# Performance work log

Hardware: AMD Instinct MI355X
Metric: run time of the kernel (lower is better)

The kernel has to match this reference:

```python
import jax, jax.numpy as jnp
import numpy as np

N = 10000      # nodes
DEG = 8        # avg out-degree before symmetrization
B = 2          # batch
T = 8          # time steps
F_IN = 1
HID = 64       # spatial hidden = temporal hidden
K = 2          # power-conv hops


def setup_inputs() -> dict:
    rng = np.random.default_rng(0)
    # random sparse adjacency, symmetrized by concatenating reversed edges
    s0 = rng.integers(0, N, size=N * DEG)
    d0 = rng.integers(0, N, size=N * DEG)
    src = np.concatenate([s0, d0]).astype(np.int32)   # [E], E = 2*N*DEG
    dst = np.concatenate([d0, s0]).astype(np.int32)
    vals = np.ones(src.shape[0], np.float32)
    # symmetric normalization: A_hat = D^{-1/2} A D^{-1/2}
    deg = np.zeros(N, np.float32)
    np.add.at(deg, dst, vals)
    dinv = 1.0 / np.sqrt(np.maximum(deg, 1.0))
    vals = (dinv[src] * dinv[dst] * vals).astype(np.float32)

    key = jax.random.key(0)
    ks = jax.random.split(key, 12)
    sc = 0.05
    return {
        "x": jax.random.normal(ks[0], (B, N, T), jnp.float32),
        "edge_src": jnp.asarray(src),
        "edge_dst": jnp.asarray(dst),
        "edge_val": jnp.asarray(vals),
        # PowerGConvDyn layer 1: F_in -> HID, K+1 power weights
        "W_sp1": jax.random.normal(ks[1], (K + 1, F_IN, HID), jnp.float32) * sc,
        "b_sp1": jnp.zeros((HID,), jnp.float32),
        # PowerGConvDyn layer 2: HID -> HID
        "W_sp2": jax.random.normal(ks[2], (K + 1, HID, HID), jnp.float32) * sc,
        "b_sp2": jnp.zeros((HID,), jnp.float32),
        # GRU (torch layout: gates stacked r,z,n)
        "W_ih": jax.random.normal(ks[3], (3 * HID, HID), jnp.float32) * sc,
        "W_hh": jax.random.normal(ks[4], (3 * HID, HID), jnp.float32) * sc,
        "b_ih": jnp.zeros((3 * HID,), jnp.float32),
        "b_hh": jnp.zeros((3 * HID,), jnp.float32),
        # head
        "W_head": jax.random.normal(ks[5], (HID, 1), jnp.float32) * sc,
        "b_head": jnp.zeros((1,), jnp.float32),
    }


def reference(x, edge_src, edge_dst, edge_val,
              W_sp1, b_sp1, W_sp2, b_sp2,
              W_ih, W_hh, b_ih, b_hh, W_head, b_head):
    Bb, Nn, Tt = x.shape
    # batch all (b,t) slices as columns: [N, B*T, F_in]
    H = x.transpose(1, 0, 2).reshape(Nn, Bb * Tt, 1)

    def spmm(Z):  # A_hat @ Z on node axis; Z: [N, M, F]
        msgs = edge_val[:, None, None] * Z[edge_src]           # [E, M, F]
        return jax.ops.segment_sum(msgs, edge_dst, num_segments=Nn)

    def power_layer(Hin, W, b):  # out = sum_k (A^k H) W_k + b, then ReLU
        out = jnp.einsum('nmf,fo->nmo', Hin, W[0])
        Z = Hin
        for k in range(1, W.shape[0]):
            Z = spmm(Z)
            out = out + jnp.einsum('nmf,fo->nmo', Z, W[k])
        return jax.nn.relu(out + b)

    H = power_layer(H, W_sp1, b_sp1)   # [N, B*T, HID]
    H = power_layer(H, W_sp2, b_sp2)   # [N, B*T, HID]
    C = H.shape[-1]

    # [N, B*T, C] -> [T, B*N, C] sequences for the GRU
    Hs = H.reshape(Nn, Bb, Tt, C).transpose(2, 1, 0, 3).reshape(Tt, Bb * Nn, C)

    Hh = W_hh.shape[1]
    h0 = jnp.zeros((Bb * Nn, Hh), x.dtype)

    def gru_step(h, xt):
        gx = xt @ W_ih.T + b_ih
        gh = h @ W_hh.T + b_hh
        rx, zx, nx = jnp.split(gx, 3, axis=-1)
        rh, zh, nh = jnp.split(gh, 3, axis=-1)
        r = jax.nn.sigmoid(rx + rh)
        z = jax.nn.sigmoid(zx + zh)
        n = jnp.tanh(nx + r * nh)
        h = (1.0 - z) * n + z * h
        return h, None

    h_last, _ = jax.lax.scan(gru_step, h0, Hs)   # [B*N, HID]
    y = (h_last @ W_head + b_head).reshape(Bb, Nn)
    return y
```

## Files before the change

kernel.cpp:

```cpp
#include <hip/hip_runtime.h>
#include <math.h>

#define N_NODES 10000
#define B_SZ 2
#define T_STEPS 8
#define M_COLS 16
#define BN 20000
#define NM 160000

typedef __attribute__((ext_vector_type(8))) short short8;
typedef __attribute__((ext_vector_type(4))) float f32x4;

__device__ __forceinline__ float b2f(unsigned short u) {
  union { unsigned int i; float f; } x; x.i = ((unsigned int)u) << 16; return x.f;
}
__device__ __forceinline__ unsigned short f2b(float f) {
  unsigned int x = __float_as_uint(f);
  return (unsigned short)((x + 0x7fffu + ((x >> 16) & 1u)) >> 16);
}
__device__ __forceinline__ float sigm(float x) {
  return 1.f / (1.f + __expf(-x));
}
__device__ __forceinline__ float tanhfast(float x) {
  float xm = fmaxf(x, -15.f);
  float e = __expf(-2.f * xm);
  return (1.f - e) / (1.f + e);
}

__global__ __launch_bounds__(256) void k_count(const int* __restrict__ dst, int* __restrict__ cnt, int E) {
  int e = blockIdx.x*256 + threadIdx.x;
  if (e < E) atomicAdd(&cnt[dst[e]], 1);
}

__global__ __launch_bounds__(256) void k_scan(const int* __restrict__ cnt, int* __restrict__ rowp, int n) {
  const int K = 40;
  int t = threadIdx.x;
  int beg = t*K;
  int end = beg + K < n ? beg + K : n;
  int s = 0;
  for (int i = beg; i < end; ++i) s += cnt[i];
  int lane = t & 63, w = t >> 6;
  int v = s;
#pragma unroll
  for (int off = 1; off < 64; off <<= 1) {
    int u = __shfl_up(v, off, 64);
    if (lane >= off) v += u;
  }
  __shared__ int wsum[4];
  if (lane == 63) wsum[w] = v;
  __syncthreads();
  int woff = 0;
  for (int i = 0; i < w; ++i) woff += wsum[i];
  int run = woff + v - s;
  for (int i = beg; i < end; ++i) { rowp[i] = run; run += cnt[i]; }
  if (t == 255) rowp[n] = run;
}

__global__ __launch_bounds__(256) void k_fill(const int* __restrict__ src, const int* __restrict__ dst,
                                              const float* __restrict__ val, const int* __restrict__ rowp,
                                              int* __restrict__ cur, int* __restrict__ csrs,
                                              float* __restrict__ csrv, int E) {
  int e = blockIdx.x*256 + threadIdx.x;
  if (e >= E) return;
  int d = dst[e];
  int p = atomicAdd(&cur[d], 1);
  int slot = rowp[d] + p;
  csrs[slot] = src[e];
  csrv[slot] = val[e];
}

__global__ __launch_bounds__(256) void k_prep(const float* __restrict__ Wih, const float* __restrict__ W2,
                                              const float* __restrict__ Whh,
                                              unsigned short* __restrict__ Wbih,
                                              unsigned short* __restrict__ W2t,
                                              unsigned short* __restrict__ Whi,
                                              unsigned short* __restrict__ Wlo) {
  int i = blockIdx.x*256 + threadIdx.x;
  if (i >= 12288) return;
  Wbih[i] = f2b(Wih[i]);
  int p = i >> 12, rem = i & 4095, c = rem >> 6, k = rem & 63;
  W2t[i] = f2b(W2[p*4096 + k*64 + c]);
  float v = Whh[i];
  unsigned short h = f2b(v);
  Whi[i] = h;
  Wlo[i] = f2b(v - b2f(h));
}

__global__ __launch_bounds__(256) void k_spmmA(const float* __restrict__ x, float* __restrict__ Z1,
                                               const int* __restrict__ rowp, const int* __restrict__ csrs,
                                               const float* __restrict__ csrv) {
  int i = blockIdx.x*256 + threadIdx.x;
  int n = i >> 4, m = i & 15;
  int b = m >> 3, t = m & 7;
  int s = rowp[n], e = rowp[n+1];
  const float* xb = x + b*(N_NODES*T_STEPS) + t;
  float acc = 0.f;
  for (int k = s; k < e; ++k)
    acc = fmaf(csrv[k], xb[csrs[k]*T_STEPS], acc);
  Z1[i] = acc;
}

__global__ __launch_bounds__(256) void k_spmmB_l1(const float* __restrict__ x, const float* __restrict__ Z1,
                                                  const int* __restrict__ rowp, const int* __restrict__ csrs,
                                                  const float* __restrict__ csrv,
                                                  const float* __restrict__ W1, const float* __restrict__ b1,
                                                  unsigned short* __restrict__ H1b) {
  int i = blockIdx.x*256 + threadIdx.x;
  int n = i >> 4, m = i & 15;
  int b = m >> 3, t = m & 7;
  int s = rowp[n], e = rowp[n+1];
  float z2 = 0.f;
  for (int k = s; k < e; ++k)
    z2 = fmaf(csrv[k], Z1[csrs[k]*16 + m], z2);
  float z0 = x[b*(N_NODES*T_STEPS) + n*T_STEPS + t];
  float z1 = Z1[i];
  unsigned short* dst = H1b + (size_t)i*64;
  union { uint4 v; unsigned short s[8]; } o;
#pragma unroll
  for (int g = 0; g < 8; ++g) {
#pragma unroll
    for (int j = 0; j < 8; ++j) {
      int c = g*8 + j;
      float v = fmaf(z0, W1[c], fmaf(z1, W1[64+c], fmaf(z2, W1[128+c], b1[c])));
      o.s[j] = f2b(v > 0.f ? v : 0.f);
    }
    ((uint4*)dst)[g] = o.v;
  }
}

__global__ __launch_bounds__(256) void k_spmmC(const unsigned short* __restrict__ Zin,
                                               unsigned short* __restrict__ Zout,
                                               const int* __restrict__ rowp, const int* __restrict__ csrs,
                                               const float* __restrict__ csrv) {
  int c = blockIdx.x & 7;
  int grp = blockIdx.x >> 3;
  int n = grp*16 + (threadIdx.x >> 4);
  int l = threadIdx.x & 15;
  int off = c*128 + l*8;
  int s = rowp[n], e = rowp[n+1];
  float acc[8] = {0,0,0,0,0,0,0,0};
  for (int k = s; k < e; ++k) {
    int src = csrs[k];
    float v = csrv[k];
    union { uint4 u; unsigned short s[8]; } z;
    z.u = *(const uint4*)(Zin + (size_t)src*1024 + off);
#pragma unroll
    for (int j = 0; j < 8; ++j) acc[j] = fmaf(v, b2f(z.s[j]), acc[j]);
  }
  union { uint4 u; unsigned short s[8]; } o;
#pragma unroll
  for (int j = 0; j < 8; ++j) o.s[j] = f2b(acc[j]);
  *(uint4*)(Zout + (size_t)n*1024 + off) = o.u;
}

__global__ __launch_bounds__(256) void k_layer2m(const unsigned short* __restrict__ H1b,
                                                 const unsigned short* __restrict__ Z1b,
                                                 const unsigned short* __restrict__ Z2b,
                                                 const unsigned short* __restrict__ Wt,
                                                 const float* __restrict__ b2,
                                                 unsigned short* __restrict__ OUT2b) {
  int wid = blockIdx.x*4 + (threadIdx.x >> 6);
  int lane = threadIdx.x & 63;
  int lr = lane & 15, hi = lane >> 4;
  int rowbase = wid*16;
  const short* A0 = (const short*)H1b + (size_t)(rowbase + lr)*64;
  const short* A1 = (const short*)Z1b + (size_t)(rowbase + lr)*64;
  const short* A2 = (const short*)Z2b + (size_t)(rowbase + lr)*64;
  short8 a[3][2];
  a[0][0] = *(const short8*)(A0 + hi*8); a[0][1] = *(const short8*)(A0 + 32 + hi*8);
  a[1][0] = *(const short8*)(A1 + hi*8); a[1][1] = *(const short8*)(A1 + 32 + hi*8);
  a[2][0] = *(const short8*)(A2 + hi*8); a[2][1] = *(const short8*)(A2 + 32 + hi*8);
  const short* Bp = (const short*)Wt;
  f32x4 acc[4];
#pragma unroll
  for (int ct = 0; ct < 4; ++ct) {
    int col = ct*16 + lr;
    f32x4 c = {0.f, 0.f, 0.f, 0.f};
#pragma unroll
    for (int p = 0; p < 3; ++p) {
      short8 b0 = *(const short8*)(Bp + p*4096 + col*64 + hi*8);
      short8 b1 = *(const short8*)(Bp + p*4096 + col*64 + 32 + hi*8);
      c = __builtin_amdgcn_mfma_f32_16x16x32_bf16(a[p][0], b0, c, 0, 0, 0);
      c = __builtin_amdgcn_mfma_f32_16x16x32_bf16(a[p][1], b1, c, 0, 0, 0);
    }
    acc[ct] = c;
  }
#pragma unroll
  for (int ct = 0; ct < 4; ++ct) {
    int col = ct*16 + lr;
    float bb = b2[col];
#pragma unroll
    for (int r = 0; r < 4; ++r) {
      int nm = rowbase + hi*4 + r;
      int n = nm >> 4, m = nm & 15;
      int bi = m >> 3, t = m & 7;
      float v = acc[ct][r] + bb;
      OUT2b[((size_t)((t*2 + bi)*N_NODES + n))*64 + col] = f2b(v > 0.f ? v : 0.f);
    }
  }
}

__global__ __launch_bounds__(256, 1) void k_gru(const unsigned short* __restrict__ OUT2b,
                                                const unsigned short* __restrict__ Whhi,
                                                const unsigned short* __restrict__ Whlo,
                                                const unsigned short* __restrict__ Wihb,
                                                const float* __restrict__ bih,
                                                const float* __restrict__ bhh,
                                                const float* __restrict__ Whead,
                                                const float* __restrict__ bhead,
                                                float* __restrict__ y) {
  extern __shared__ char smem[];
  uint4* WF = (uint4*)smem;
  float* HSb = (float*)(smem + 73728);
  int tid = threadIdx.x;
  for (int idx = tid; idx < 72*64; idx += 256) {
    int f = idx >> 6, ln = idx & 63;
    int lrr = ln & 15, h4r = ln >> 4;
    int g = (f < 24) ? f : ((f < 48) ? f - 24 : f - 48);
    int ct = g >> 1, kc = g & 1;
    const unsigned short* src = (f < 24) ? Whhi : ((f < 48) ? Whlo : Wihb);
    WF[idx] = *(const uint4*)(src + (ct*16 + lrr)*64 + kc*32 + h4r*8);
  }
  int w = tid >> 6, lane = tid & 63;
  int lr = lane & 15, h4 = lane >> 4;
  float* hs = HSb + w*(16*68);
  for (int i = lane; i < 16*68; i += 64) hs[i] = 0.f;
  __syncthreads();
  int Wv = blockIdx.x*4 + w;
  if (Wv >= 1250) return;
  int base = Wv*16;
  int row0 = base + lr;
  int b0 = row0 >= N_NODES ? 1 : 0;
  int n0 = row0 - b0*N_NODES;

  float cR[4], cZ[4], bNi[4], bNh[4];
#pragma unroll
  for (int cr = 0; cr < 4; ++cr) {
    int col = cr*16 + lr;
    cR[cr]  = bih[col] + bhh[col];
    cZ[cr]  = bih[64+col] + bhh[64+col];
    bNi[cr] = bih[128+col];
    bNh[cr] = bhh[128+col];
  }
  float hreg[4][4];
#pragma unroll
  for (int cr = 0; cr < 4; ++cr)
#pragma unroll
    for (int j = 0; j < 4; ++j) hreg[cr][j] = 0.f;
  const short* O = (const short*)OUT2b;

#pragma unroll 1
  for (int t = 0; t < 8; ++t) {
    short8 ax[2];
    size_t ab0 = ((size_t)((t*2 + b0)*N_NODES + n0))*64;
#pragma unroll
    for (int kc = 0; kc < 2; ++kc)
      ax[kc] = *(const short8*)(O + ab0 + kc*32 + h4*8);
    short8 ahi[2], alo[2];
#pragma unroll
    for (int kc = 0; kc < 2; ++kc) {
      const float* hp = hs + lr*68 + kc*32 + h4*8;
      float4 v0 = *(const float4*)hp;
      float4 v1 = *(const float4*)(hp + 4);
      float hv[8];
      hv[0]=v0.x; hv[1]=v0.y; hv[2]=v0.z; hv[3]=v0.w;
      hv[4]=v1.x; hv[5]=v1.y; hv[6]=v1.z; hv[7]=v1.w;
      union { short8 v; unsigned short s[8]; } uh, ul;
#pragma unroll
      for (int j = 0; j < 8; ++j) {
        unsigned short hb = (unsigned short)(__float_as_uint(hv[j]) >> 16);
        uh.s[j] = hb;
        ul.s[j] = f2b(hv[j] - b2f(hb));
      }
      ahi[kc] = uh.v; alo[kc] = ul.v;
    }
    f32x4 aR[4], aZ[4], aNx[4], aNh[4];
#pragma unroll
    for (int cr = 0; cr < 4; ++cr) {
      f32x4 zz = {0.f,0.f,0.f,0.f};
      aR[cr] = zz; aZ[cr] = zz; aNx[cr] = zz; aNh[cr] = zz;
    }
#pragma unroll
    for (int ct = 0; ct < 12; ++ct) {
#pragma unroll
      for (int kc = 0; kc < 2; ++kc) {
        short8 bhi = *(const short8*)&WF[(ct*2 + kc)*64 + lane];
        short8 blo = *(const short8*)&WF[(24 + ct*2 + kc)*64 + lane];
        short8 bx  = *(const short8*)&WF[(48 + ct*2 + kc)*64 + lane];
        if (ct < 4) {
          aR[ct] = __builtin_amdgcn_mfma_f32_16x16x32_bf16(ax[kc],  bx,  aR[ct], 0, 0, 0);
          aR[ct] = __builtin_amdgcn_mfma_f32_16x16x32_bf16(ahi[kc], bhi, aR[ct], 0, 0, 0);
          aR[ct] = __builtin_amdgcn_mfma_f32_16x16x32_bf16(ahi[kc], blo, aR[ct], 0, 0, 0);
          aR[ct] = __builtin_amdgcn_mfma_f32_16x16x32_bf16(alo[kc], bhi, aR[ct], 0, 0, 0);
        } else if (ct < 8) {
          int cc = ct - 4;
          aZ[cc] = __builtin_amdgcn_mfma_f32_16x16x32_bf16(ax[kc],  bx,  aZ[cc], 0, 0, 0);
          aZ[cc] = __builtin_amdgcn_mfma_f32_16x16x32_bf16(ahi[kc], bhi, aZ[cc], 0, 0, 0);
          aZ[cc] = __builtin_amdgcn_mfma_f32_16x16x32_bf16(ahi[kc], blo, aZ[cc], 0, 0, 0);
          aZ[cc] = __builtin_amdgcn_mfma_f32_16x16x32_bf16(alo[kc], bhi, aZ[cc], 0, 0, 0);
        } else {
          int cc = ct - 8;
          aNx[cc] = __builtin_amdgcn_mfma_f32_16x16x32_bf16(ax[kc],  bx,  aNx[cc], 0, 0, 0);
          aNh[cc] = __builtin_amdgcn_mfma_f32_16x16x32_bf16(ahi[kc], bhi, aNh[cc], 0, 0, 0);
          aNh[cc] = __builtin_amdgcn_mfma_f32_16x16x32_bf16(ahi[kc], blo, aNh[cc], 0, 0, 0);
          aNh[cc] = __builtin_amdgcn_mfma_f32_16x16x32_bf16(alo[kc], bhi, aNh[cc], 0, 0, 0);
        }
      }
    }
#pragma unroll
    for (int cr = 0; cr < 4; ++cr)
#pragma unroll
      for (int j = 0; j < 4; ++j) {
        float r = sigm(aR[cr][j] + cR[cr]);
        float z = sigm(aZ[cr][j] + cZ[cr]);
        float nn = tanhfast(aNx[cr][j] + bNi[cr] + r*(aNh[cr][j] + bNh[cr]));
        float hv = (1.f - z)*nn + z*hreg[cr][j];
        hreg[cr][j] = hv;
        hs[(h4*4 + j)*68 + cr*16 + lr] = hv;
      }
  }
  float wv[4];
#pragma unroll
  for (int cr = 0; cr < 4; ++cr) wv[cr] = Whead[cr*16 + lr];
#pragma unroll
  for (int j = 0; j < 4; ++j) {
    float p = 0.f;
#pragma unroll
    for (int cr = 0; cr < 4; ++cr) p = fmaf(hreg[j >= 0 ? cr : 0][j], wv[cr], p);
#pragma unroll
    for (int off = 1; off <= 8; off <<= 1)
      p += __shfl_xor(p, off, 64);
    if (lr == 0) y[base + h4*4 + j] = p + bhead[0];
  }
}

extern "C" void kernel_launch(void* const* d_in, const int* in_sizes, int n_in,
                              void* d_out, int out_size, void* d_ws, size_t ws_size,
                              hipStream_t stream) {
  const float* x    = (const float*)d_in[0];
  const int*   esrc = (const int*)d_in[1];
  const int*   edst = (const int*)d_in[2];
  const float* eval = (const float*)d_in[3];
  const float* W1   = (const float*)d_in[4];
  const float* b1   = (const float*)d_in[5];
  const float* W2   = (const float*)d_in[6];
  const float* b2   = (const float*)d_in[7];
  const float* Wih  = (const float*)d_in[8];
  const float* Whh  = (const float*)d_in[9];
  const float* bih  = (const float*)d_in[10];
  const float* bhh  = (const float*)d_in[11];
  const float* Whead= (const float*)d_in[12];
  const float* bhead= (const float*)d_in[13];
  int E = in_sizes[1];
  float* y = (float*)d_out;

  char* wsb = (char*)d_ws;
  unsigned short* H1b   = (unsigned short*)(wsb + 0);
  unsigned short* ZB1   = (unsigned short*)(wsb + 20480000);
  unsigned short* ZB2   = (unsigned short*)(wsb + 40960000);
  unsigned short* OUT2b = (unsigned short*)(wsb + 61440000);
  float* Z1   = (float*)(wsb + 82560000);
  int*   rowp = (int*)(wsb + 83840000);
  int*   cnt  = (int*)(wsb + 83880064);
  int*   csrs = (int*)(wsb + 83920064);
  float* csrv = (float*)(wsb + 84560064);
  unsigned short* Wbih = (unsigned short*)(wsb + 85200064);
  unsigned short* W2t  = (unsigned short*)(wsb + 85224640);
  unsigned short* Whhi = (unsigned short*)(wsb + 85249280);
  unsigned short* Whlo = (unsigned short*)(wsb + 85273856);

  int eb = (E + 255) / 256;

  hipMemsetAsync(cnt, 0, N_NODES*sizeof(int), stream);
  k_count<<<eb, 256, 0, stream>>>(edst, cnt, E);
  k_scan<<<1, 256, 0, stream>>>(cnt, rowp, N_NODES);
  hipMemsetAsync(cnt, 0, N_NODES*sizeof(int), stream);
  k_fill<<<eb, 256, 0, stream>>>(esrc, edst, eval, rowp, cnt, csrs, csrv, E);
  k_prep<<<48, 256, 0, stream>>>(Wih, W2, Whh, Wbih, W2t, Whhi, Whlo);

  k_spmmA<<<625, 256, 0, stream>>>(x, Z1, rowp, csrs, csrv);
  k_spmmB_l1<<<625, 256, 0, stream>>>(x, Z1, rowp, csrs, csrv, W1, b1, H1b);

  k_spmmC<<<5000, 256, 0, stream>>>(H1b, ZB1, rowp, csrs, csrv);
  k_spmmC<<<5000, 256, 0, stream>>>(ZB1, ZB2, rowp, csrs, csrv);
  k_layer2m<<<2500, 256, 0, stream>>>(H1b, ZB1, ZB2, W2t, b2, OUT2b);

  const int gru_lds = 73728 + 4*16*68*4;
  hipFuncSetAttribute((const void*)k_gru, hipFuncAttributeMaxDynamicSharedMemorySize, gru_lds);
  k_gru<<<313, 256, gru_lds, stream>>>(OUT2b, Whhi, Whlo, Wbih, bih, bhh, Whead, bhead, y);
}
```

Measured before the change: 270.5 us.

## Split GRU gates across three waves per 16-row tile with register-resident W_hh

The GRU kernel now gives each 16-row tile its own 192-thread block. Each of the three waves computes one gate (r, z or n), instead of one wave computing all three gates for its rows. The recurrent weight hi/lo fragments stay in registers, so only W_ih goes to LDS, which cuts LDS use and lets more blocks run per CU. The r and z pre-activations are exchanged through LDS to the n-gate wave, which does the nonlinearity and state update. This costs two block barriers per time step, and two of the three waves sit idle during the elementwise phase.

```diff
diff --git a/kernel.cpp b/kernel.cpp
--- a/kernel.cpp
+++ b/kernel.cpp
@@ -200,7 +200,7 @@
   }
 }
 
-__global__ __launch_bounds__(256, 1) void k_gru(const unsigned short* __restrict__ OUT2b,
+__global__ __launch_bounds__(192, 2) void k_gru(const unsigned short* __restrict__ OUT2b,
                                                 const unsigned short* __restrict__ Whhi,
                                                 const unsigned short* __restrict__ Whlo,
                                                 const unsigned short* __restrict__ Wihb,
@@ -210,37 +210,41 @@
                                                 const float* __restrict__ bhead,
                                                 float* __restrict__ y) {
   extern __shared__ char smem[];
-  uint4* WF = (uint4*)smem;
-  float* HSb = (float*)(smem + 73728);
+  uint4* WX  = (uint4*)smem;
+  float* hs  = (float*)(smem + 24576);
+  float* gex = (float*)(smem + 24576 + 4864);
   int tid = threadIdx.x;
-  for (int idx = tid; idx < 72*64; idx += 256) {
+  for (int idx = tid; idx < 24*64; idx += 192) {
     int f = idx >> 6, ln = idx & 63;
     int lrr = ln & 15, h4r = ln >> 4;
-    int g = (f < 24) ? f : ((f < 48) ? f - 24 : f - 48);
-    int ct = g >> 1, kc = g & 1;
-    const unsigned short* src = (f < 24) ? Whhi : ((f < 48) ? Whlo : Wihb);
-    WF[idx] = *(const uint4*)(src + (ct*16 + lrr)*64 + kc*32 + h4r*8);
-  }
-  int w = tid >> 6, lane = tid & 63;
-  int lr = lane & 15, h4 = lane >> 4;
-  float* hs = HSb + w*(16*68);
-  for (int i = lane; i < 16*68; i += 64) hs[i] = 0.f;
-  __syncthreads();
-  int Wv = blockIdx.x*4 + w;
-  if (Wv >= 1250) return;
-  int base = Wv*16;
+    int ct = f >> 1, kc = f & 1;
+    WX[idx] = *(const uint4*)(Wihb + (ct*16 + lrr)*64 + kc*32 + h4r*8);
+  }
+  for (int i = tid; i < 16*76; i += 192) hs[i] = 0.f;
+  int w = __builtin_amdgcn_readfirstlane(tid >> 6);
+  int lane = tid & 63, lr = lane & 15, h4 = lane >> 4;
+  int base = blockIdx.x*16;
   int row0 = base + lr;
   int b0 = row0 >= N_NODES ? 1 : 0;
   int n0 = row0 - b0*N_NODES;
 
-  float cR[4], cZ[4], bNi[4], bNh[4];
+  const unsigned short* Whp = Whhi;
+  const unsigned short* Wlp = Whlo;
+  short8 wh[4][2], wl[4][2];
+#pragma unroll
+  for (int ct = 0; ct < 4; ++ct)
+#pragma unroll
+    for (int kc = 0; kc < 2; ++kc) {
+      int col = w*64 + ct*16 + lr;
+      wh[ct][kc] = *(const short8*)((const short*)Whp + col*64 + kc*32 + h4*8);
+      wl[ct][kc] = *(const short8*)((const short*)Wlp + col*64 + kc*32 + h4*8);
+    }
+  float c0[4], c1[4];
 #pragma unroll
   for (int cr = 0; cr < 4; ++cr) {
-    int col = cr*16 + lr;
-    cR[cr]  = bih[col] + bhh[col];
-    cZ[cr]  = bih[64+col] + bhh[64+col];
-    bNi[cr] = bih[128+col];
-    bNh[cr] = bhh[128+col];
+    int col = w*64 + cr*16 + lr;
+    if (w < 2) { c0[cr] = bih[col] + bhh[col]; c1[cr] = 0.f; }
+    else       { c0[cr] = bih[col];            c1[cr] = bhh[col]; }
   }
   float hreg[4][4];
 #pragma unroll
@@ -248,18 +252,25 @@
 #pragma unroll
     for (int j = 0; j < 4; ++j) hreg[cr][j] = 0.f;
   const short* O = (const short*)OUT2b;
+  __syncthreads();
 
 #pragma unroll 1
   for (int t = 0; t < 8; ++t) {
+#pragma unroll
+    for (int ct = 0; ct < 4; ++ct)
+#pragma unroll
+      for (int kc = 0; kc < 2; ++kc) {
+        asm volatile("" : "+v"(wh[ct][kc]));
+        asm volatile("" : "+v"(wl[ct][kc]));
+      }
     short8 ax[2];
     size_t ab0 = ((size_t)((t*2 + b0)*N_NODES + n0))*64;
-#pragma unroll
-    for (int kc = 0; kc < 2; ++kc)
-      ax[kc] = *(const short8*)(O + ab0 + kc*32 + h4*8);
+    ax[0] = *(const short8*)(O + ab0 + h4*8);
+    ax[1] = *(const short8*)(O + ab0 + 32 + h4*8);
     short8 ahi[2], alo[2];
 #pragma unroll
     for (int kc = 0; kc < 2; ++kc) {
-      const float* hp = hs + lr*68 + kc*32 + h4*8;
+      const float* hp = hs + lr*76 + kc*32 + h4*8;
       float4 v0 = *(const float4*)hp;
       float4 v1 = *(const float4*)(hp + 4);
       float hv[8];
@@ -274,63 +285,70 @@
       }
       ahi[kc] = uh.v; alo[kc] = ul.v;
     }
-    f32x4 aR[4], aZ[4], aNx[4], aNh[4];
+    f32x4 accA[4], accB[4];
 #pragma unroll
     for (int cr = 0; cr < 4; ++cr) {
       f32x4 zz = {0.f,0.f,0.f,0.f};
-      aR[cr] = zz; aZ[cr] = zz; aNx[cr] = zz; aNh[cr] = zz;
-    }
-#pragma unroll
-    for (int ct = 0; ct < 12; ++ct) {
+      accA[cr] = zz; accB[cr] = zz;
+    }
+#pragma unroll
+    for (int ct = 0; ct < 4; ++ct) {
 #pragma unroll
       for (int kc = 0; kc < 2; ++kc) {
-        short8 bhi = *(const short8*)&WF[(ct*2 + kc)*64 + lane];
-        short8 blo = *(const short8*)&WF[(24 + ct*2 + kc)*64 + lane];
-        short8 bx  = *(const short8*)&WF[(48 + ct*2 + kc)*64 + lane];
-        if (ct < 4) {
-          aR[ct] = __builtin_amdgcn_mfma_f32_16x16x32_bf16(ax[kc],  bx,  aR[ct], 0, 0, 0);
-          aR[ct] = __builtin_amdgcn_mfma_f32_16x16x32_bf16(ahi[kc], bhi, aR[ct], 0, 0, 0);
-          aR[ct] = __builtin_amdgcn_mfma_f32_16x16x32_bf16(ahi[kc], blo, aR[ct], 0, 0, 0);
-          aR[ct] = __builtin_amdgcn_mfma_f32_16x16x32_bf16(alo[kc], bhi, aR[ct], 0, 0, 0);
-        } else if (ct < 8) {
-          int cc = ct - 4;
-          aZ[cc] = __builtin_amdgcn_mfma_f32_16x16x32_bf16(ax[kc],  bx,  aZ[cc], 0, 0, 0);
-          aZ[cc] = __builtin_amdgcn_mfma_f32_16x16x32_bf16(ahi[kc], bhi, aZ[cc], 0, 0, 0);
-          aZ[cc] = __builtin_amdgcn_mfma_f32_16x16x32_bf16(ahi[kc], blo, aZ[cc], 0, 0, 0);
-          aZ[cc] = __builtin_amdgcn_mfma_f32_16x16x32_bf16(alo[kc], bhi, aZ[cc], 0, 0, 0);
+        short8 bx = *(const short8*)&WX[(w*8 + ct*2 + kc)*64 + lane];
+        if (w < 2) {
+          accA[ct] = __builtin_amdgcn_mfma_f32_16x16x32_bf16(ax[kc],  bx,         accA[ct], 0, 0, 0);
+          accA[ct] = __builtin_amdgcn_mfma_f32_16x16x32_bf16(ahi[kc], wh[ct][kc], accA[ct], 0, 0, 0);
+          accA[ct] = __builtin_amdgcn_mfma_f32_16x16x32_bf16(ahi[kc], wl[ct][kc], accA[ct], 0, 0, 0);
+          accA[ct] = __builtin_amdgcn_mfma_f32_16x16x32_bf16(alo[kc], wh[ct][kc], accA[ct], 0, 0, 0);
         } else {
-          int cc = ct - 8;
-          aNx[cc] = __builtin_amdgcn_mfma_f32_16x16x32_bf16(ax[kc],  bx,  aNx[cc], 0, 0, 0);
-          aNh[cc] = __builtin_amdgcn_mfma_f32_16x16x32_bf16(ahi[kc], bhi, aNh[cc], 0, 0, 0);
-          aNh[cc] = __builtin_amdgcn_mfma_f32_16x16x32_bf16(ahi[kc], blo, aNh[cc], 0, 0, 0);
-          aNh[cc] = __builtin_amdgcn_mfma_f32_16x16x32_bf16(alo[kc], bhi, aNh[cc], 0, 0, 0);
+          accA[ct] = __builtin_amdgcn_mfma_f32_16x16x32_bf16(ax[kc],  bx,         accA[ct], 0, 0, 0);
+          accB[ct] = __builtin_amdgcn_mfma_f32_16x16x32_bf16(ahi[kc], wh[ct][kc], accB[ct], 0, 0, 0);
+          accB[ct] = __builtin_amdgcn_mfma_f32_16x16x32_bf16(ahi[kc], wl[ct][kc], accB[ct], 0, 0, 0);
+          accB[ct] = __builtin_amdgcn_mfma_f32_16x16x32_bf16(alo[kc], wh[ct][kc], accB[ct], 0, 0, 0);
         }
       }
     }
-#pragma unroll
-    for (int cr = 0; cr < 4; ++cr)
-#pragma unroll
-      for (int j = 0; j < 4; ++j) {
-        float r = sigm(aR[cr][j] + cR[cr]);
-        float z = sigm(aZ[cr][j] + cZ[cr]);
-        float nn = tanhfast(aNx[cr][j] + bNi[cr] + r*(aNh[cr][j] + bNh[cr]));
-        float hv = (1.f - z)*nn + z*hreg[cr][j];
-        hreg[cr][j] = hv;
-        hs[(h4*4 + j)*68 + cr*16 + lr] = hv;
-      }
-  }
-  float wv[4];
-#pragma unroll
-  for (int cr = 0; cr < 4; ++cr) wv[cr] = Whead[cr*16 + lr];
-#pragma unroll
-  for (int j = 0; j < 4; ++j) {
-    float p = 0.f;
-#pragma unroll
-    for (int cr = 0; cr < 4; ++cr) p = fmaf(hreg[j >= 0 ? cr : 0][j], wv[cr], p);
-#pragma unroll
-    for (int off = 1; off <= 8; off <<= 1)
-      p += __shfl_xor(p, off, 64);
-    if (lr == 0) y[base + h4*4 + j] = p + bhead[0];
+    if (w < 2) {
+#pragma unroll
+      for (int cr = 0; cr < 4; ++cr)
+#pragma unroll
+        for (int j = 0; j < 4; ++j)
+          gex[(w*16 + cr*4 + j)*64 + lane] = accA[cr][j] + c0[cr];
+    }
+    __syncthreads();
+    if (w == 2) {
+#pragma unroll
+      for (int cr = 0; cr < 4; ++cr)
+#pragma unroll
+        for (int j = 0; j < 4; ++j) {
+          float rv = gex[(cr*4 + j)*64 + lane];
+          float zv = gex[(16 + cr*4 + j)*64 + lane];
+          float r = sigm(rv);
+          float z = sigm(zv);
+          float nn = tanhfast(accA[cr][j] + c0[cr] + r*(accB[cr][j] + c1[cr]));
+          float hv = (1.f - z)*nn + z*hreg[cr][j];
+          hreg[cr][j] = hv;
+          hs[(h4*4 + j)*76 + cr*16 + lr] = hv;
+        }
+    }
+    __syncthreads();
+  }
+  if (w == 2) {
+    float wv[4];
+#pragma unroll
+    for (int cr = 0; cr < 4; ++cr) wv[cr] = Whead[cr*16 + lr];
+#pragma unroll
+    for (int j = 0; j < 4; ++j) {
+      float p = 0.f;
+#pragma unroll
+      for (int cr = 0; cr < 4; ++cr) p = fmaf(hreg[cr][j], wv[cr], p);
+      p += __shfl_xor(p, 1, 64);
+      p += __shfl_xor(p, 2, 64);
+      p += __shfl_xor(p, 4, 64);
+      p += __shfl_xor(p, 8, 64);
+      if (lr == 0) y[base + h4*4 + j] = p + bhead[0];
+    }
   }
 }
 
@@ -385,7 +403,7 @@
   k_spmmC<<<5000, 256, 0, stream>>>(ZB1, ZB2, rowp, csrs, csrv);
   k_layer2m<<<2500, 256, 0, stream>>>(H1b, ZB1, ZB2, W2t, b2, OUT2b);
 
-  const int gru_lds = 73728 + 4*16*68*4;
+  const int gru_lds = 24576 + 16*76*4 + 2*16*64*4;
   hipFuncSetAttribute((const void*)k_gru, hipFuncAttributeMaxDynamicSharedMemorySize, gru_lds);
-  k_gru<<<313, 256, gru_lds, stream>>>(OUT2b, Whhi, Whlo, Wbih, bih, bhh, Whead, bhead, y);
-}
+  k_gru<<<1250, 192, gru_lds, stream>>>(OUT2b, Whhi, Whlo, Wbih, bih, bhh, Whead, bhead, y);
+}
```

Result: slower. 292.7 us (+8.2%).

## Enlarge GRU blocks to 12 waves, keep input weights in registers, fuse memset into scan

Applied to the files above, without the earlier changes.

The GRU kernel now runs 768-thread blocks (12 waves) instead of 4 waves. The W_ih bf16 fragments move from LDS into per-lane registers, which shrinks the LDS weight region so more waves share one copy of W_hh hi/lo. The second memset of the counter array is folded into the scan kernel, removing one API call. The hi part of the hidden-state split now uses round-to-nearest instead of truncation, and the head reduction loop is written out by hand. Holding 24 short8 weight fragments per lane raises register pressure and may hurt occupancy or cause spills; the grid also drops to 105 blocks.

```diff
diff --git a/kernel.cpp b/kernel.cpp
--- a/kernel.cpp
+++ b/kernel.cpp
@@ -32,13 +32,14 @@
   if (e < E) atomicAdd(&cnt[dst[e]], 1);
 }
 
-__global__ __launch_bounds__(256) void k_scan(const int* __restrict__ cnt, int* __restrict__ rowp, int n) {
+__global__ __launch_bounds__(256) void k_scan(const int* __restrict__ cntin, int* __restrict__ rowp,
+                                              int* __restrict__ cntz, int n) {
   const int K = 40;
   int t = threadIdx.x;
   int beg = t*K;
   int end = beg + K < n ? beg + K : n;
   int s = 0;
-  for (int i = beg; i < end; ++i) s += cnt[i];
+  for (int i = beg; i < end; ++i) s += cntin[i];
   int lane = t & 63, w = t >> 6;
   int v = s;
 #pragma unroll
@@ -52,7 +53,11 @@
   int woff = 0;
   for (int i = 0; i < w; ++i) woff += wsum[i];
   int run = woff + v - s;
-  for (int i = beg; i < end; ++i) { rowp[i] = run; run += cnt[i]; }
+  for (int i = beg; i < end; ++i) {
+    rowp[i] = run;
+    run += cntin[i];
+    cntz[i] = 0;
+  }
   if (t == 255) rowp[n] = run;
 }
 
@@ -200,7 +205,7 @@
   }
 }
 
-__global__ __launch_bounds__(256, 1) void k_gru(const unsigned short* __restrict__ OUT2b,
+__global__ __launch_bounds__(768, 3) void k_gru(const unsigned short* __restrict__ OUT2b,
                                                 const unsigned short* __restrict__ Whhi,
                                                 const unsigned short* __restrict__ Whlo,
                                                 const unsigned short* __restrict__ Wihb,
@@ -211,14 +216,14 @@
                                                 float* __restrict__ y) {
   extern __shared__ char smem[];
   uint4* WF = (uint4*)smem;
-  float* HSb = (float*)(smem + 73728);
+  float* HSb = (float*)(smem + 49152);
   int tid = threadIdx.x;
-  for (int idx = tid; idx < 72*64; idx += 256) {
+  for (int idx = tid; idx < 48*64; idx += 768) {
     int f = idx >> 6, ln = idx & 63;
     int lrr = ln & 15, h4r = ln >> 4;
-    int g = (f < 24) ? f : ((f < 48) ? f - 24 : f - 48);
+    int g = (f < 24) ? f : f - 24;
     int ct = g >> 1, kc = g & 1;
-    const unsigned short* src = (f < 24) ? Whhi : ((f < 48) ? Whlo : Wihb);
+    const unsigned short* src = (f < 24) ? Whhi : Whlo;
     WF[idx] = *(const uint4*)(src + (ct*16 + lrr)*64 + kc*32 + h4r*8);
   }
   int w = tid >> 6, lane = tid & 63;
@@ -226,12 +231,20 @@
   float* hs = HSb + w*(16*68);
   for (int i = lane; i < 16*68; i += 64) hs[i] = 0.f;
   __syncthreads();
-  int Wv = blockIdx.x*4 + w;
+  int Wv = blockIdx.x*12 + w;
   if (Wv >= 1250) return;
   int base = Wv*16;
   int row0 = base + lr;
   int b0 = row0 >= N_NODES ? 1 : 0;
   int n0 = row0 - b0*N_NODES;
+
+  const short* Wx = (const short*)Wihb;
+  short8 wx[12][2];
+#pragma unroll
+  for (int ct = 0; ct < 12; ++ct)
+#pragma unroll
+    for (int kc = 0; kc < 2; ++kc)
+      wx[ct][kc] = *(const short8*)(Wx + (ct*16 + lr)*64 + kc*32 + h4*8);
 
   float cR[4], cZ[4], bNi[4], bNh[4];
 #pragma unroll
@@ -268,7 +281,7 @@
       union { short8 v; unsigned short s[8]; } uh, ul;
 #pragma unroll
       for (int j = 0; j < 8; ++j) {
-        unsigned short hb = (unsigned short)(__float_as_uint(hv[j]) >> 16);
+        unsigned short hb = f2b(hv[j]);
         uh.s[j] = hb;
         ul.s[j] = f2b(hv[j] - b2f(hb));
       }
@@ -286,24 +299,23 @@
       for (int kc = 0; kc < 2; ++kc) {
         short8 bhi = *(const short8*)&WF[(ct*2 + kc)*64 + lane];
         short8 blo = *(const short8*)&WF[(24 + ct*2 + kc)*64 + lane];
-        short8 bx  = *(const short8*)&WF[(48 + ct*2 + kc)*64 + lane];
         if (ct < 4) {
-          aR[ct] = __builtin_amdgcn_mfma_f32_16x16x32_bf16(ax[kc],  bx,  aR[ct], 0, 0, 0);
-          aR[ct] = __builtin_amdgcn_mfma_f32_16x16x32_bf16(ahi[kc], bhi, aR[ct], 0, 0, 0);
-          aR[ct] = __builtin_amdgcn_mfma_f32_16x16x32_bf16(ahi[kc], blo, aR[ct], 0, 0, 0);
-          aR[ct] = __builtin_amdgcn_mfma_f32_16x16x32_bf16(alo[kc], bhi, aR[ct], 0, 0, 0);
+          aR[ct] = __builtin_amdgcn_mfma_f32_16x16x32_bf16(ax[kc],  wx[ct][kc], aR[ct], 0, 0, 0);
+          aR[ct] = __builtin_amdgcn_mfma_f32_16x16x32_bf16(ahi[kc], bhi,        aR[ct], 0, 0, 0);
+          aR[ct] = __builtin_amdgcn_mfma_f32_16x16x32_bf16(ahi[kc], blo,        aR[ct], 0, 0, 0);
+          aR[ct] = __builtin_amdgcn_mfma_f32_16x16x32_bf16(alo[kc], bhi,        aR[ct], 0, 0, 0);
         } else if (ct < 8) {
           int cc = ct - 4;
-          aZ[cc] = __builtin_amdgcn_mfma_f32_16x16x32_bf16(ax[kc],  bx,  aZ[cc], 0, 0, 0);
-          aZ[cc] = __builtin_amdgcn_mfma_f32_16x16x32_bf16(ahi[kc], bhi, aZ[cc], 0, 0, 0);
-          aZ[cc] = __builtin_amdgcn_mfma_f32_16x16x32_bf16(ahi[kc], blo, aZ[cc], 0, 0, 0);
-          aZ[cc] = __builtin_amdgcn_mfma_f32_16x16x32_bf16(alo[kc], bhi, aZ[cc], 0, 0, 0);
+          aZ[cc] = __builtin_amdgcn_mfma_f32_16x16x32_bf16(ax[kc],  wx[ct][kc], aZ[cc], 0, 0, 0);
+          aZ[cc] = __builtin_amdgcn_mfma_f32_16x16x32_bf16(ahi[kc], bhi,        aZ[cc], 0, 0, 0);
+          aZ[cc] = __builtin_amdgcn_mfma_f32_16x16x32_bf16(ahi[kc], blo,        aZ[cc], 0, 0, 0);
+          aZ[cc] = __builtin_amdgcn_mfma_f32_16x16x32_bf16(alo[kc], bhi,        aZ[cc], 0, 0, 0);
         } else {
           int cc = ct - 8;
-          aNx[cc] = __builtin_amdgcn_mfma_f32_16x16x32_bf16(ax[kc],  bx,  aNx[cc], 0, 0, 0);
-          aNh[cc] = __builtin_amdgcn_mfma_f32_16x16x32_bf16(ahi[kc], bhi, aNh[cc], 0, 0, 0);
-          aNh[cc] = __builtin_amdgcn_mfma_f32_16x16x32_bf16(ahi[kc], blo, aNh[cc], 0, 0, 0);
-          aNh[cc] = __builtin_amdgcn_mfma_f32_16x16x32_bf16(alo[kc], bhi, aNh[cc], 0, 0, 0);
+          aNx[cc] = __builtin_amdgcn_mfma_f32_16x16x32_bf16(ax[kc],  wx[ct][kc], aNx[cc], 0, 0, 0);
+          aNh[cc] = __builtin_amdgcn_mfma_f32_16x16x32_bf16(ahi[kc], bhi,        aNh[cc], 0, 0, 0);
+          aNh[cc] = __builtin_amdgcn_mfma_f32_16x16x32_bf16(ahi[kc], blo,        aNh[cc], 0, 0, 0);
+          aNh[cc] = __builtin_amdgcn_mfma_f32_16x16x32_bf16(alo[kc], bhi,        aNh[cc], 0, 0, 0);
         }
       }
     }
@@ -326,10 +338,11 @@
   for (int j = 0; j < 4; ++j) {
     float p = 0.f;
 #pragma unroll
-    for (int cr = 0; cr < 4; ++cr) p = fmaf(hreg[j >= 0 ? cr : 0][j], wv[cr], p);
-#pragma unroll
-    for (int off = 1; off <= 8; off <<= 1)
-      p += __shfl_xor(p, off, 64);
+    for (int cr = 0; cr < 4; ++cr) p = fmaf(hreg[cr][j], wv[cr], p);
+    p += __shfl_xor(p, 1, 64);
+    p += __shfl_xor(p, 2, 64);
+    p += __shfl_xor(p, 4, 64);
+    p += __shfl_xor(p, 8, 64);
     if (lr == 0) y[base + h4*4 + j] = p + bhead[0];
   }
 }
@@ -373,8 +386,7 @@
 
   hipMemsetAsync(cnt, 0, N_NODES*sizeof(int), stream);
   k_count<<<eb, 256, 0, stream>>>(edst, cnt, E);
-  k_scan<<<1, 256, 0, stream>>>(cnt, rowp, N_NODES);
-  hipMemsetAsync(cnt, 0, N_NODES*sizeof(int), stream);
+  k_scan<<<1, 256, 0, stream>>>(cnt, rowp, cnt, N_NODES);
   k_fill<<<eb, 256, 0, stream>>>(esrc, edst, eval, rowp, cnt, csrs, csrv, E);
   k_prep<<<48, 256, 0, stream>>>(Wih, W2, Whh, Wbih, W2t, Whhi, Whlo);
 
@@ -385,7 +397,7 @@
   k_spmmC<<<5000, 256, 0, stream>>>(ZB1, ZB2, rowp, csrs, csrv);
   k_layer2m<<<2500, 256, 0, stream>>>(H1b, ZB1, ZB2, W2t, b2, OUT2b);
 
-  const int gru_lds = 73728 + 4*16*68*4;
+  const int gru_lds = 49152 + 12*16*68*4;
   hipFuncSetAttribute((const void*)k_gru, hipFuncAttributeMaxDynamicSharedMemorySize, gru_lds);
-  k_gru<<<313, 256, gru_lds, stream>>>(OUT2b, Whhi, Whlo, Wbih, bih, bhh, Whead, bhead, y);
-}
+  k_gru<<<105, 768, gru_lds, stream>>>(OUT2b, Whhi, Whlo, Wbih, bih, bhh, Whead, bhead, y);
+}
```

Measured after the change: 292.0 us. 1.08x slower.
